# Optimization experiments

Measured on AMD Instinct MI355X. Metric: run time of the kernel, lower is better.

Reference implementation:

```python
import jax, jax.numpy as jnp
import numpy as np

N = 30000
E = 600000
IN = 64
HID = 128
EPS = 1e-5
HEADS_PER_LAYER = (4, 4, 1)


def _bn(x, g, b):
    # eval-mode BatchNorm: running_mean=0, running_var=1
    return x * (g / np.sqrt(1.0 + EPS)) + b


def _segment_softmax(e, dst, n):
    m = jax.ops.segment_max(e, dst, num_segments=n)
    ex = jnp.exp(e - m[dst])
    s = jax.ops.segment_sum(ex, dst, num_segments=n)
    return ex / (s[dst] + 1e-16)


def _gcn_conv(x, w, b, src, dst, norm, n):
    m = (x @ w)[src] * norm[:, None]            # [E+N, HID]
    return jax.ops.segment_sum(m, dst, num_segments=n) + b


def _gat_conv(x, w, a_src, a_dst, b, src, dst, n, heads):
    C = HID // heads
    xh = (x @ w).reshape(n, heads, C)
    asrc = (xh * a_src.reshape(heads, C)).sum(-1)   # [N, heads]
    adst = (xh * a_dst.reshape(heads, C)).sum(-1)
    e = jax.nn.leaky_relu(asrc[src] + adst[dst], 0.2)  # [E+N, heads]
    alpha = _segment_softmax(e, dst, n)
    out = jax.ops.segment_sum(xh[src] * alpha[:, :, None], dst, num_segments=n)
    return out.reshape(n, HID) + b


def _forward(x, gcn_in_w, gcn_in_b, gcn_res_w, gcn_res_b, gcn_w, gcn_b,
             gcn_bn_g, gcn_bn_b, gcn_c1w, gcn_c1b, gcn_c2w, gcn_c2b,
             gcn_c3w, gcn_c3b, gat_in_w, gat_in_b, gat_w, gat_asrc,
             gat_adst, gat_b, gat_bn_g, gat_bn_b, feat_imp, gat_c1w,
             gat_c1b, gat_cbn_g, gat_cbn_b, gat_c2w, gat_c2b, gat_c3w,
             gat_c3b, fin_w, fin_b, fin_bn_g, fin_bn_b, fin2_w, fin2_b,
             edge_index):
    n = x.shape[0]
    loop = jnp.arange(n, dtype=edge_index.dtype)
    src = jnp.concatenate([edge_index[0], loop])  # add self-loops
    dst = jnp.concatenate([edge_index[1], loop])
    # GCN symmetric normalization (with self-loops)
    deg = jax.ops.segment_sum(jnp.ones_like(dst, dtype=x.dtype), dst, num_segments=n)
    dis = jnp.where(deg > 0, jax.lax.rsqrt(jnp.maximum(deg, 1.0)), 0.0)
    norm = dis[src] * dis[dst]

    # ---- GCN branch (eval: dropout = identity, self-attn skipped since N>5000) ----
    xp = x @ gcn_in_w + gcn_in_b
    res = x @ gcn_res_w + gcn_res_b
    for i in range(3):
        xn = _gcn_conv(xp, gcn_w[i], gcn_b[i], src, dst, norm, n)
        xn = jax.nn.relu(_bn(xn, gcn_bn_g[i], gcn_bn_b[i]))
        if i % 2 == 1:
            xp = xn + res
            res = xp
        else:
            xp = xn
    h = jax.nn.relu(xp @ gcn_c1w + gcn_c1b)
    h = jax.nn.relu(h @ gcn_c2w + gcn_c2b)
    gcn_out = h @ gcn_c3w + gcn_c3b

    # ---- GAT branch ----
    xg = x @ gat_in_w + gat_in_b
    for i in range(3):
        xg = _gat_conv(xg, gat_w[i], gat_asrc[i], gat_adst[i], gat_b[i],
                       src, dst, n, HEADS_PER_LAYER[i])
        xg = jax.nn.elu(_bn(xg, gat_bn_g[i], gat_bn_b[i]))
    xg = xg * feat_imp
    h = jax.nn.relu(xg @ gat_c1w + gat_c1b)
    h = _bn(h, gat_cbn_g, gat_cbn_b)
    h = jax.nn.relu(h @ gat_c2w + gat_c2b)
    gat_out = h @ gat_c3w + gat_c3b

    # ---- fusion: N > 10000 -> weighted blend path ----
    fused = 0.6 * gcn_out + 0.4 * gat_out
    h = jax.nn.relu(fused @ fin_w + fin_b)
    h = _bn(h, fin_bn_g, fin_bn_b)
    return h @ fin2_w + fin2_b  # [N, 2]


def setup_inputs() -> dict:
    key = jax.random.key(0)
    ks = iter(jax.random.split(key, 64))

    def nrm(shape, scale=1.0):
        return jax.random.normal(next(ks), shape, dtype=jnp.float32) * scale

    s_in = 1.0 / np.sqrt(IN)
    s_h = 1.0 / np.sqrt(HID)
    inp = {}
    inp['x'] = nrm((N, IN))
    inp['edge_index'] = jax.random.randint(next(ks), (2, E), 0, N, dtype=jnp.int32)
    inp['gcn_in_w'] = nrm((IN, HID), s_in); inp['gcn_in_b'] = nrm((HID,), 0.01)
    inp['gcn_res_w'] = nrm((IN, HID), s_in); inp['gcn_res_b'] = nrm((HID,), 0.01)
    inp['gcn_w'] = nrm((3, HID, HID), s_h); inp['gcn_b'] = nrm((3, HID), 0.01)
    inp['gcn_bn_g'] = 1.0 + nrm((3, HID), 0.1); inp['gcn_bn_b'] = nrm((3, HID), 0.1)
    inp['gcn_c1w'] = nrm((HID, 64), s_h); inp['gcn_c1b'] = nrm((64,), 0.01)
    inp['gcn_c2w'] = nrm((64, 32), 0.125); inp['gcn_c2b'] = nrm((32,), 0.01)
    inp['gcn_c3w'] = nrm((32, HID), 0.18); inp['gcn_c3b'] = nrm((HID,), 0.01)
    inp['gat_in_w'] = nrm((IN, HID), s_in); inp['gat_in_b'] = nrm((HID,), 0.01)
    inp['gat_w'] = nrm((3, HID, HID), s_h)
    inp['gat_asrc'] = nrm((3, HID), s_h); inp['gat_adst'] = nrm((3, HID), s_h)
    inp['gat_b'] = nrm((3, HID), 0.01)
    inp['gat_bn_g'] = 1.0 + nrm((3, HID), 0.1); inp['gat_bn_b'] = nrm((3, HID), 0.1)
    inp['feat_imp'] = 1.0 + nrm((HID,), 0.1)
    inp['gat_c1w'] = nrm((HID, 64), s_h); inp['gat_c1b'] = nrm((64,), 0.01)
    inp['gat_cbn_g'] = 1.0 + nrm((64,), 0.1); inp['gat_cbn_b'] = nrm((64,), 0.1)
    inp['gat_c2w'] = nrm((64, 32), 0.125); inp['gat_c2b'] = nrm((32,), 0.01)
    inp['gat_c3w'] = nrm((32, HID), 0.18); inp['gat_c3b'] = nrm((HID,), 0.01)
    inp['fin_w'] = nrm((HID, 64), s_h); inp['fin_b'] = nrm((64,), 0.01)
    inp['fin_bn_g'] = 1.0 + nrm((64,), 0.1); inp['fin_bn_b'] = nrm((64,), 0.1)
    inp['fin2_w'] = nrm((64, 2), 0.125); inp['fin2_b'] = nrm((2,), 0.01)
    return inp


def reference(x, edge_index, gcn_in_w, gcn_in_b, gcn_res_w, gcn_res_b, gcn_w,
              gcn_b, gcn_bn_g, gcn_bn_b, gcn_c1w, gcn_c1b, gcn_c2w, gcn_c2b,
              gcn_c3w, gcn_c3b, gat_in_w, gat_in_b, gat_w, gat_asrc, gat_adst,
              gat_b, gat_bn_g, gat_bn_b, feat_imp, gat_c1w, gat_c1b, gat_cbn_g,
              gat_cbn_b, gat_c2w, gat_c2b, gat_c3w, gat_c3b, fin_w, fin_b,
              fin_bn_g, fin_bn_b, fin2_w, fin2_b):
    return _forward(x, gcn_in_w, gcn_in_b, gcn_res_w, gcn_res_b, gcn_w, gcn_b,
                    gcn_bn_g, gcn_bn_b, gcn_c1w, gcn_c1b, gcn_c2w, gcn_c2b,
                    gcn_c3w, gcn_c3b, gat_in_w, gat_in_b, gat_w, gat_asrc,
                    gat_adst, gat_b, gat_bn_g, gat_bn_b, feat_imp, gat_c1w,
                    gat_c1b, gat_cbn_g, gat_cbn_b, gat_c2w, gat_c2b, gat_c3w,
                    gat_c3b, fin_w, fin_b, fin_bn_g, fin_bn_b, fin2_w, fin2_b,
                    edge_index)
```

## Files before the change

kernel.cpp:

```cpp
#include <hip/hip_runtime.h>
#include <hip/hip_fp16.h>

#define RSQ_BN 0.9999950000374997f

typedef _Float16 f16x8 __attribute__((ext_vector_type(8)));
typedef float f32x4 __attribute__((ext_vector_type(4)));

union H8u { uint4 u4; __half h[8]; };

__device__ __forceinline__ float leaky02(float x) { return x > 0.f ? x : 0.2f * x; }

__device__ __forceinline__ float4 ld4(const float* p) {
    return *reinterpret_cast<const float4*>(p);
}
__device__ __forceinline__ void st4(float* p, float4 v) {
    *reinterpret_cast<float4*>(p) = v;
}
__device__ __forceinline__ void ld8(float* d, const float* p) {
    float4 u = ld4(p), v = ld4(p + 4);
    d[0] = u.x; d[1] = u.y; d[2] = u.z; d[3] = u.w;
    d[4] = v.x; d[5] = v.y; d[6] = v.z; d[7] = v.w;
}
__device__ __forceinline__ void st8(float* p, const float* v) {
    st4(p, make_float4(v[0], v[1], v[2], v[3]));
    st4(p + 4, make_float4(v[4], v[5], v[6], v[7]));
}


__global__ void hist_k(const int* __restrict__ edst, int* __restrict__ cnt, int E, int EN) {
    int i = blockIdx.x * 256 + threadIdx.x;
    if (i >= EN) return;
    int d = (i < E) ? edst[i] : (i - E);
    atomicAdd(&cnt[d], 1);
}

__global__ __launch_bounds__(256)
void scanA_k(const int* __restrict__ cnt, int* __restrict__ rowptr,
             int* __restrict__ bsum, int n) {
    __shared__ int sh[256];
    int t = threadIdx.x;
    int i = blockIdx.x * 256 + t;
    int v = (i < n) ? cnt[i] : 0;
    sh[t] = v;
    __syncthreads();
#pragma unroll
    for (int off = 1; off < 256; off <<= 1) {
        int u = 0;
        if (t >= off) u = sh[t - off];
        __syncthreads();
        sh[t] += u;
        __syncthreads();
    }
    if (i < n) rowptr[i] = sh[t] - v;
    if (t == 255) bsum[blockIdx.x] = sh[255];
}

__global__ __launch_bounds__(256)
void scanB_k(int* __restrict__ bsum, int nb) {
    __shared__ int sh[256];
    int t = threadIdx.x;
    int v = (t < nb) ? bsum[t] : 0;
    sh[t] = v;
    __syncthreads();
#pragma unroll
    for (int off = 1; off < 256; off <<= 1) {
        int u = 0;
        if (t >= off) u = sh[t - off];
        __syncthreads();
        sh[t] += u;
        __syncthreads();
    }
    if (t < nb) bsum[t] = sh[t] - v;
}

__global__ __launch_bounds__(256)
void scanC_k(const int* __restrict__ cnt, const int* __restrict__ bsum,
             int* __restrict__ rowptr, int* __restrict__ cursor,
             float* __restrict__ dis, int n, int EN) {
    int i = blockIdx.x * 256 + threadIdx.x;
    if (i < n) {
        int r = rowptr[i] + bsum[blockIdx.x];
        rowptr[i] = r;
        cursor[i] = r;
        dis[i] = rsqrtf((float)cnt[i]);
    }
    if (i == 0) rowptr[n] = EN;
}

__global__ void scatter_k(const int* __restrict__ esrc, const int* __restrict__ edst,
                          int* __restrict__ cursor, int* __restrict__ colidx, int E, int EN) {
    int i = blockIdx.x * 256 + threadIdx.x;
    if (i >= EN) return;
    int s, d;
    if (i < E) { s = esrc[i]; d = edst[i]; }
    else       { s = i - E; d = s; }
    int pos = atomicAdd(&cursor[d], 1);
    colidx[pos] = s;
}


__global__ void wtx_all_k(const float* __restrict__ gcn_in_w, const float* __restrict__ gcn_res_w,
                          const float* __restrict__ gat_in_w,
                          const float* __restrict__ gcn_w, const float* __restrict__ gat_w,
                          const float* __restrict__ gcn_c1w, const float* __restrict__ gat_c1w,
                          const float* __restrict__ gcn_c3w, const float* __restrict__ gat_c3w,
                          const float* __restrict__ fin_w,
                          const float* __restrict__ gcn_c2w, const float* __restrict__ gat_c2w,
                          __half* __restrict__ WTin, __half* __restrict__ WTg,
                          __half* __restrict__ WTa, __half* __restrict__ WTc1,
                          __half* __restrict__ WTc3, __half* __restrict__ WTfin,
                          __half* __restrict__ WTc2) {
    int idx = blockIdx.x * 256 + threadIdx.x;
    const float* src;
    __half* dst;
    int K, M, o;
    if (idx < 24576) {
        int mi = idx >> 13; o = idx & 8191;
        src = mi == 0 ? gcn_in_w : (mi == 1 ? gcn_res_w : gat_in_w);
        dst = WTin + mi * 8192; K = 64; M = 128;
    } else if (idx < 73728) {
        int r = idx - 24576; int mi = r >> 14; o = r & 16383;
        src = gcn_w + mi * 16384; dst = WTg + mi * 16384; K = 128; M = 128;
    } else if (idx < 122880) {
        int r = idx - 73728; int mi = r >> 14; o = r & 16383;
        src = gat_w + mi * 16384; dst = WTa + mi * 16384; K = 128; M = 128;
    } else if (idx < 139264) {
        int r = idx - 122880; int mi = r >> 13; o = r & 8191;
        src = mi ? gat_c1w : gcn_c1w; dst = WTc1 + mi * 8192; K = 128; M = 64;
    } else if (idx < 147456) {
        int r = idx - 139264; int mi = r >> 12; o = r & 4095;
        src = mi ? gat_c3w : gcn_c3w; dst = WTc3 + mi * 4096; K = 32; M = 128;
    } else if (idx < 155648) {
        o = idx - 147456; src = fin_w; dst = WTfin; K = 128; M = 64;
    } else if (idx < 159744) {
        int r = idx - 155648; int mi = r >> 11; o = r & 2047;
        src = mi ? gat_c2w : gcn_c2w; dst = WTc2 + mi * 2048; K = 64; M = 32;
    } else return;
    int mcol = o / K, k = o - mcol * K;
    dst[o] = (__half)src[k * M + mcol];
}


__device__ __forceinline__ f16x8 mk_af(const float* xr, int kb) {
    float4 v0 = ld4(xr + kb), v1 = ld4(xr + kb + 4);
    f16x8 af;
    af[0] = (_Float16)v0.x; af[1] = (_Float16)v0.y;
    af[2] = (_Float16)v0.z; af[3] = (_Float16)v0.w;
    af[4] = (_Float16)v1.x; af[5] = (_Float16)v1.y;
    af[6] = (_Float16)v1.z; af[7] = (_Float16)v1.w;
    return af;
}

__global__ __launch_bounds__(256)
void mfma_lin3_k(const float* __restrict__ X, const __half* __restrict__ WTin,
                 const float* __restrict__ b0, float* __restrict__ Y0,
                 const float* __restrict__ b1, float* __restrict__ Y1,
                 const float* __restrict__ b2, float* __restrict__ Y2,
                 int n, int gper) {
    constexpr int K = 64, CT = 8;
    int set = blockIdx.x / gper, blk = blockIdx.x % gper;
    const __half* WT = WTin + (size_t)set * 8192;
    const float* bi = set == 0 ? b0 : (set == 1 ? b1 : b2);
    float* Y = set == 0 ? Y0 : (set == 1 ? Y1 : Y2);
    int wave = threadIdx.x >> 6, lane = threadIdx.x & 63;
    int m = lane & 15, quad = lane >> 4;
    int row0 = blk * 64 + wave * 16;
    int arow = min(row0 + m, n - 1);
    const float* xr = X + (size_t)arow * K;
    f32x4 acc[CT];
#pragma unroll
    for (int ct = 0; ct < CT; ++ct) acc[ct] = (f32x4){0.f, 0.f, 0.f, 0.f};
#pragma unroll
    for (int k32 = 0; k32 < K / 32; ++k32) {
        int kb = k32 * 32 + quad * 8;
        f16x8 af = mk_af(xr, kb);
#pragma unroll
        for (int ct = 0; ct < CT; ++ct) {
            f16x8 bf = *reinterpret_cast<const f16x8*>(WT + (size_t)(ct * 16 + m) * K + kb);
            acc[ct] = __builtin_amdgcn_mfma_f32_16x16x32_f16(af, bf, acc[ct], 0, 0, 0);
        }
    }
#pragma unroll
    for (int ct = 0; ct < CT; ++ct) {
        int col = ct * 16 + m;
        float cb = bi[col];
#pragma unroll
        for (int reg = 0; reg < 4; ++reg) {
            int row = row0 + quad * 4 + reg;
            if (row < n) Y[(size_t)row * 128 + col] = acc[ct][reg] + cb;
        }
    }
}


__global__ __launch_bounds__(256)
void dual128_mfma_k(const float* __restrict__ Xg, const __half* __restrict__ WTg,
                    __half* __restrict__ Yg,
                    const float* __restrict__ Xa, const __half* __restrict__ WTa,
                    __half* __restrict__ Ya,
                    const float* __restrict__ dis,
                    const float* __restrict__ asrc, const float* __restrict__ adst,
                    float* __restrict__ avp, float* __restrict__ bvp,
                    int hh, int n, int gper) {
    bool gat = blockIdx.x >= gper;
    int blk = gat ? blockIdx.x - gper : blockIdx.x;
    const float* X = gat ? Xa : Xg;
    const __half* WT = gat ? WTa : WTg;
    __half* Y = gat ? Ya : Yg;
    int wave = threadIdx.x >> 6;
    int lane = threadIdx.x & 63;
    int m = lane & 15, quad = lane >> 4;
    int row0 = blk * 64 + wave * 16;
    int arow = min(row0 + m, n - 1);
    const float* xr = X + (size_t)arow * 128;
    f32x4 acc[8];
#pragma unroll
    for (int ct = 0; ct < 8; ++ct) acc[ct] = (f32x4){0.f, 0.f, 0.f, 0.f};
#pragma unroll
    for (int k32 = 0; k32 < 4; ++k32) {
        int kb = k32 * 32 + quad * 8;
        f16x8 af = mk_af(xr, kb);
#pragma unroll
        for (int ct = 0; ct < 8; ++ct) {
            f16x8 bf = *reinterpret_cast<const f16x8*>(WT + (size_t)(ct * 16 + m) * 128 + kb);
            acc[ct] = __builtin_amdgcn_mfma_f32_16x16x32_f16(af, bf, acc[ct], 0, 0, 0);
        }
    }
    if (!gat) {
#pragma unroll
        for (int reg = 0; reg < 4; ++reg) {
            int row = row0 + quad * 4 + reg;
            if (row < n) {
                float dv = dis[row];
#pragma unroll
                for (int ct = 0; ct < 8; ++ct)
                    Y[(size_t)row * 128 + ct * 16 + m] = (__half)(acc[ct][reg] * dv);
            }
        }
    } else {
        float cas[8], cad[8];
#pragma unroll
        for (int ct = 0; ct < 8; ++ct) {
            cas[ct] = asrc[ct * 16 + m];
            cad[ct] = adst[ct * 16 + m];
        }
        int ctph = 8 / hh;
#pragma unroll
        for (int reg = 0; reg < 4; ++reg) {
            int row = row0 + quad * 4 + reg;
            bool valid = row < n;
            if (valid) {
#pragma unroll
                for (int ct = 0; ct < 8; ++ct)
                    Y[(size_t)row * 128 + ct * 16 + m] = (__half)acc[ct][reg];
            }
            for (int h = 0; h < hh; ++h) {
                float sa = 0.f, sd = 0.f;
                for (int j = 0; j < ctph; ++j) {
                    int ct = h * ctph + j;
                    sa += acc[ct][reg] * cas[ct];
                    sd += acc[ct][reg] * cad[ct];
                }
                for (int off = 1; off < 16; off <<= 1) {
                    sa += __shfl_xor(sa, off);
                    sd += __shfl_xor(sd, off);
                }
                if (m == 0 && valid) {
                    avp[row * hh + h] = sa;
                    bvp[row * hh + h] = sd;
                }
            }
        }
    }
}


__global__ __launch_bounds__(256)
void fused_gather_k(const int* __restrict__ rowptr, const int* __restrict__ colidx,
                    const float* __restrict__ dis,
                    const __half* __restrict__ Tg, const float* __restrict__ gbias,
                    const float* __restrict__ gbng, const float* __restrict__ gbnb,
                    const float* __restrict__ res, float* __restrict__ Yg,
                    const __half* __restrict__ Ta, const float* __restrict__ avp,
                    const float* __restrict__ bvp, const float* __restrict__ abias,
                    const float* __restrict__ abng, const float* __restrict__ abnb,
                    const float* __restrict__ fimp, float* __restrict__ Ya,
                    int n, int hh, int log2C) {
    int idx = blockIdx.x * 256 + threadIdx.x;
    int i = idx >> 4;
    if (i >= n) return;
    int c = (idx & 15) * 8;
    int h = c >> log2C;
    float ad = bvp[i * hh + h];
    int p0 = rowptr[i], p1 = rowptr[i + 1];
    float g[8], a[8];
#pragma unroll
    for (int t = 0; t < 8; ++t) { g[t] = 0.f; a[t] = 0.f; }
    float m = -3.0e38f, s = 0.f;

    int p = p0;
    int nfull = (p1 - p0) >> 2;
    int sx[4]; float av[4];
    if (nfull > 0) {
#pragma unroll
        for (int j = 0; j < 4; ++j) sx[j] = colidx[p + j];
#pragma unroll
        for (int j = 0; j < 4; ++j) av[j] = avp[sx[j] * hh + h];
    }
    for (int gi = 0; gi < nfull; ++gi) {
        uint4 qg[4], qa[4];
#pragma unroll
        for (int j = 0; j < 4; ++j)
            qg[j] = *reinterpret_cast<const uint4*>(Tg + (size_t)sx[j] * 128 + c);
#pragma unroll
        for (int j = 0; j < 4; ++j)
            qa[j] = *reinterpret_cast<const uint4*>(Ta + (size_t)sx[j] * 128 + c);
        int pn = p + 4;
        bool more = (gi + 1) < nfull;
        int sn[4]; float avn[4];
#pragma unroll
        for (int j = 0; j < 4; ++j) sn[j] = more ? colidx[pn + j] : 0;
#pragma unroll
        for (int j = 0; j < 4; ++j) avn[j] = avp[sn[j] * hh + h];
        float e0 = leaky02(av[0] + ad), e1 = leaky02(av[1] + ad);
        float e2 = leaky02(av[2] + ad), e3 = leaky02(av[3] + ad);
        float mc = fmaxf(fmaxf(e0, e1), fmaxf(e2, e3));
        float mn = fmaxf(m, mc);
        float scale = __expf(m - mn);
        float w0 = __expf(e0 - mn), w1 = __expf(e1 - mn);
        float w2 = __expf(e2 - mn), w3 = __expf(e3 - mn);
        s = s * scale + (w0 + w1 + w2 + w3);
        m = mn;
        {
            H8u k0, k1, k2, k3;
            k0.u4 = qg[0]; k1.u4 = qg[1]; k2.u4 = qg[2]; k3.u4 = qg[3];
#pragma unroll
            for (int t = 0; t < 8; ++t)
                g[t] += __half2float(k0.h[t]) + __half2float(k1.h[t])
                      + __half2float(k2.h[t]) + __half2float(k3.h[t]);
        }
        {
            H8u k0, k1, k2, k3;
            k0.u4 = qa[0]; k1.u4 = qa[1]; k2.u4 = qa[2]; k3.u4 = qa[3];
#pragma unroll
            for (int t = 0; t < 8; ++t) {
                float v = a[t] * scale;
                v = fmaf(__half2float(k0.h[t]), w0, v);
                v = fmaf(__half2float(k1.h[t]), w1, v);
                v = fmaf(__half2float(k2.h[t]), w2, v);
                v = fmaf(__half2float(k3.h[t]), w3, v);
                a[t] = v;
            }
        }
        p = pn;
#pragma unroll
        for (int j = 0; j < 4; ++j) { sx[j] = sn[j]; av[j] = avn[j]; }
    }
    for (; p < p1; ++p) {
        int s0 = colidx[p];
        float e0 = leaky02(avp[s0 * hh + h] + ad);
        uint4 qg0 = *reinterpret_cast<const uint4*>(Tg + (size_t)s0 * 128 + c);
        uint4 qa0 = *reinterpret_cast<const uint4*>(Ta + (size_t)s0 * 128 + c);
        float mn = fmaxf(m, e0);
        float scale = __expf(m - mn);
        float w0 = __expf(e0 - mn);
        s = s * scale + w0;
        m = mn;
        H8u kg, ka; kg.u4 = qg0; ka.u4 = qa0;
#pragma unroll
        for (int t = 0; t < 8; ++t) {
            g[t] += __half2float(kg.h[t]);
            a[t] = fmaf(__half2float(ka.h[t]), w0, a[t] * scale);
        }
    }

    {
        float di = dis[i];
        float bb[8], gg[8], nb[8];
        ld8(bb, gbias + c); ld8(gg, gbng + c); ld8(nb, gbnb + c);
        float o[8];
#pragma unroll
        for (int t = 0; t < 8; ++t) {
            float v = g[t] * di + bb[t];
            o[t] = fmaxf(v * (gg[t] * RSQ_BN) + nb[t], 0.f);
        }
        if (res) {
            float rr[8]; ld8(rr, res + (size_t)i * 128 + c);
#pragma unroll
            for (int t = 0; t < 8; ++t) o[t] += rr[t];
        }
        st8(Yg + (size_t)i * 128 + c, o);
    }
    {
        float si = 1.f / (s + 1e-16f);
        float bb[8], gg[8], nb[8];
        ld8(bb, abias + c); ld8(gg, abng + c); ld8(nb, abnb + c);
        float o[8];
#pragma unroll
        for (int t = 0; t < 8; ++t) {
            float v = a[t] * si + bb[t];
            v = v * (gg[t] * RSQ_BN) + nb[t];
            o[t] = v > 0.f ? v : expm1f(v);
        }
        if (fimp) {
            float ff[8]; ld8(ff, fimp + c);
#pragma unroll
            for (int t = 0; t < 8; ++t) o[t] *= ff[t];
        }
        st8(Ya + (size_t)i * 128 + c, o);
    }
}


__global__ __launch_bounds__(256)
void fused_tail_k(const float* __restrict__ Xg, const float* __restrict__ Xa,
                  const __half* __restrict__ WTc1,
                  const float* __restrict__ c1bg, const float* __restrict__ c1ba,
                  const float* __restrict__ cbng, const float* __restrict__ cbnb,
                  const __half* __restrict__ WTc2,
                  const float* __restrict__ c2bg, const float* __restrict__ c2ba,
                  const __half* __restrict__ WTc3,
                  const float* __restrict__ c3bg, const float* __restrict__ c3ba,
                  const __half* __restrict__ WTfin, const float* __restrict__ finb,
                  const float* __restrict__ fbng, const float* __restrict__ fbnb,
                  const float* __restrict__ w2, const float* __restrict__ b2,
                  float* __restrict__ out, int n) {
    __shared__ alignas(16) __half h1s[2][64][88];
    __shared__ alignas(16) __half h2s[2][64][56];
    __shared__ alignas(16) __half Fs[64][152];
    int wave = threadIdx.x >> 6, lane = threadIdx.x & 63;
    int m = lane & 15, quad = lane >> 4;
    int row0 = blockIdx.x * 64 + wave * 16;
    int lr0 = wave * 16;
    int arow = min(row0 + m, n - 1);

#pragma unroll
    for (int br = 0; br < 2; ++br) {
        const float* xr = (br ? Xa : Xg) + (size_t)arow * 128;
        const __half* WT = WTc1 + br * 8192;
        f32x4 acc[4];
#pragma unroll
        for (int ct = 0; ct < 4; ++ct) acc[ct] = (f32x4){0.f, 0.f, 0.f, 0.f};
#pragma unroll
        for (int k32 = 0; k32 < 4; ++k32) {
            int kb = k32 * 32 + quad * 8;
            f16x8 af = mk_af(xr, kb);
#pragma unroll
            for (int ct = 0; ct < 4; ++ct) {
                f16x8 bf = *reinterpret_cast<const f16x8*>(WT + (ct * 16 + m) * 128 + kb);
                acc[ct] = __builtin_amdgcn_mfma_f32_16x16x32_f16(af, bf, acc[ct], 0, 0, 0);
            }
        }
        const float* bi = br ? c1ba : c1bg;
#pragma unroll
        for (int ct = 0; ct < 4; ++ct) {
            int col = ct * 16 + m;
            float cb = bi[col];
            float cg = br ? cbng[col] * RSQ_BN : 1.f;
            float cbb = br ? cbnb[col] : 0.f;
#pragma unroll
            for (int reg = 0; reg < 4; ++reg) {
                float v = fmaxf(acc[ct][reg] + cb, 0.f) * cg + cbb;
                h1s[br][lr0 + quad * 4 + reg][col] = (__half)v;
            }
        }
    }
    __syncthreads();
#pragma unroll
    for (int br = 0; br < 2; ++br) {
        f32x4 acc[2];
        acc[0] = (f32x4){0.f, 0.f, 0.f, 0.f};
        acc[1] = (f32x4){0.f, 0.f, 0.f, 0.f};
        const __half* WT = WTc2 + br * 2048;
#pragma unroll
        for (int k32 = 0; k32 < 2; ++k32) {
            int kb = k32 * 32 + quad * 8;
            f16x8 af = *reinterpret_cast<const f16x8*>(&h1s[br][lr0 + m][kb]);
#pragma unroll
            for (int ct = 0; ct < 2; ++ct) {
                f16x8 bf = *reinterpret_cast<const f16x8*>(WT + (ct * 16 + m) * 64 + kb);
                acc[ct] = __builtin_amdgcn_mfma_f32_16x16x32_f16(af, bf, acc[ct], 0, 0, 0);
            }
        }
        const float* bi = br ? c2ba : c2bg;
#pragma unroll
        for (int ct = 0; ct < 2; ++ct) {
            int col = ct * 16 + m;
            float cb = bi[col];
#pragma unroll
            for (int reg = 0; reg < 4; ++reg) {
                float v = fmaxf(acc[ct][reg] + cb, 0.f);
                h2s[br][lr0 + quad * 4 + reg][col] = (__half)v;
            }
        }
    }
    __syncthreads();
    {
        f32x4 ag[8], aa[8];
#pragma unroll
        for (int ct = 0; ct < 8; ++ct) {
            ag[ct] = (f32x4){0.f, 0.f, 0.f, 0.f};
            aa[ct] = (f32x4){0.f, 0.f, 0.f, 0.f};
        }
        int kb = quad * 8;
        f16x8 afg = *reinterpret_cast<const f16x8*>(&h2s[0][lr0 + m][kb]);
        f16x8 afa = *reinterpret_cast<const f16x8*>(&h2s[1][lr0 + m][kb]);
#pragma unroll
        for (int ct = 0; ct < 8; ++ct) {
            f16x8 bfg = *reinterpret_cast<const f16x8*>(WTc3 + (ct * 16 + m) * 32 + kb);
            f16x8 bfa = *reinterpret_cast<const f16x8*>(WTc3 + 4096 + (ct * 16 + m) * 32 + kb);
            ag[ct] = __builtin_amdgcn_mfma_f32_16x16x32_f16(afg, bfg, ag[ct], 0, 0, 0);
            aa[ct] = __builtin_amdgcn_mfma_f32_16x16x32_f16(afa, bfa, aa[ct], 0, 0, 0);
        }
#pragma unroll
        for (int ct = 0; ct < 8; ++ct) {
            int col = ct * 16 + m;
            float cb = 0.6f * c3bg[col] + 0.4f * c3ba[col];
#pragma unroll
            for (int reg = 0; reg < 4; ++reg) {
                float v = 0.6f * ag[ct][reg] + 0.4f * aa[ct][reg] + cb;
                Fs[lr0 + quad * 4 + reg][col] = (__half)v;
            }
        }
    }
    __syncthreads();
    {
        f32x4 acc[4];
#pragma unroll
        for (int ct = 0; ct < 4; ++ct) acc[ct] = (f32x4){0.f, 0.f, 0.f, 0.f};
#pragma unroll
        for (int k32 = 0; k32 < 4; ++k32) {
            int kb = k32 * 32 + quad * 8;
            f16x8 af = *reinterpret_cast<const f16x8*>(&Fs[lr0 + m][kb]);
#pragma unroll
            for (int ct = 0; ct < 4; ++ct) {
                f16x8 bf = *reinterpret_cast<const f16x8*>(WTfin + (ct * 16 + m) * 128 + kb);
                acc[ct] = __builtin_amdgcn_mfma_f32_16x16x32_f16(af, bf, acc[ct], 0, 0, 0);
            }
        }
        float p0[4] = {0.f, 0.f, 0.f, 0.f}, p1[4] = {0.f, 0.f, 0.f, 0.f};
#pragma unroll
        for (int ct = 0; ct < 4; ++ct) {
            int col = ct * 16 + m;
            float cb = finb[col];
            float cg = fbng[col] * RSQ_BN;
            float cbb = fbnb[col];
            float w20 = w2[2 * col], w21 = w2[2 * col + 1];
#pragma unroll
            for (int reg = 0; reg < 4; ++reg) {
                float v = fmaxf(acc[ct][reg] + cb, 0.f) * cg + cbb;
                p0[reg] += v * w20;
                p1[reg] += v * w21;
            }
        }
        for (int off = 1; off < 16; off <<= 1) {
#pragma unroll
            for (int reg = 0; reg < 4; ++reg) {
                p0[reg] += __shfl_xor(p0[reg], off);
                p1[reg] += __shfl_xor(p1[reg], off);
            }
        }
        if (m == 0) {
#pragma unroll
            for (int reg = 0; reg < 4; ++reg) {
                int row = row0 + quad * 4 + reg;
                if (row < n) {
                    out[row * 2] = p0[reg] + b2[0];
                    out[row * 2 + 1] = p1[reg] + b2[1];
                }
            }
        }
    }
}


static inline int cdiv(int a, int b) { return (a + b - 1) / b; }

extern "C" void kernel_launch(void* const* d_in, const int* in_sizes, int n_in,
                              void* d_out, int out_size, void* d_ws, size_t ws_size,
                              hipStream_t stream) {
    const float* x       = (const float*)d_in[0];
    const int*   ei      = (const int*)d_in[1];
    const float* gcn_in_w = (const float*)d_in[2];
    const float* gcn_in_b = (const float*)d_in[3];
    const float* gcn_res_w = (const float*)d_in[4];
    const float* gcn_res_b = (const float*)d_in[5];
    const float* gcn_w   = (const float*)d_in[6];
    const float* gcn_b   = (const float*)d_in[7];
    const float* gcn_bn_g = (const float*)d_in[8];
    const float* gcn_bn_b = (const float*)d_in[9];
    const float* gcn_c1w = (const float*)d_in[10];
    const float* gcn_c1b = (const float*)d_in[11];
    const float* gcn_c2w = (const float*)d_in[12];
    const float* gcn_c2b = (const float*)d_in[13];
    const float* gcn_c3w = (const float*)d_in[14];
    const float* gcn_c3b = (const float*)d_in[15];
    const float* gat_in_w = (const float*)d_in[16];
    const float* gat_in_b = (const float*)d_in[17];
    const float* gat_w   = (const float*)d_in[18];
    const float* gat_asrc = (const float*)d_in[19];
    const float* gat_adst = (const float*)d_in[20];
    const float* gat_b   = (const float*)d_in[21];
    const float* gat_bn_g = (const float*)d_in[22];
    const float* gat_bn_b = (const float*)d_in[23];
    const float* feat_imp = (const float*)d_in[24];
    const float* gat_c1w = (const float*)d_in[25];
    const float* gat_c1b = (const float*)d_in[26];
    const float* gat_cbn_g = (const float*)d_in[27];
    const float* gat_cbn_b = (const float*)d_in[28];
    const float* gat_c2w = (const float*)d_in[29];
    const float* gat_c2b = (const float*)d_in[30];
    const float* gat_c3w = (const float*)d_in[31];
    const float* gat_c3b = (const float*)d_in[32];
    const float* fin_w   = (const float*)d_in[33];
    const float* fin_b   = (const float*)d_in[34];
    const float* fin_bn_g = (const float*)d_in[35];
    const float* fin_bn_b = (const float*)d_in[36];
    const float* fin2_w  = (const float*)d_in[37];
    const float* fin2_b  = (const float*)d_in[38];

    const int N = in_sizes[0] / 64;
    const int E = in_sizes[1] / 2;
    const int EN = E + N;
    const int* esrc = ei;
    const int* edst = ei + E;

    char* wp = (char*)d_ws;
    auto alloc = [&](size_t bytes) -> void* {
        void* p = (void*)wp;
        wp += (bytes + 255) & ~(size_t)255;
        return p;
    };
    int* cnt    = (int*)alloc((size_t)N * 4);
    int* rowptr = (int*)alloc((size_t)(N + 1) * 4);
    int* cursor = (int*)alloc((size_t)N * 4);
    int* bsum   = (int*)alloc((size_t)256 * 4);
    int* colidx = (int*)alloc((size_t)EN * 4);
    float* dis  = (float*)alloc((size_t)N * 4);
    float* A    = (float*)alloc((size_t)N * 128 * 4);
    float* B    = (float*)alloc((size_t)N * 128 * 4);
    float* G    = (float*)alloc((size_t)N * 128 * 4);
    float* H    = (float*)alloc((size_t)N * 128 * 4);
    float* R    = (float*)alloc((size_t)N * 128 * 4);
    __half* Th1 = (__half*)alloc((size_t)N * 128 * 2);
    __half* Th2 = (__half*)alloc((size_t)N * 128 * 2);
    float* avv  = (float*)alloc((size_t)N * 4 * 4);
    float* bvv  = (float*)alloc((size_t)N * 4 * 4);
    __half* WTin = (__half*)alloc((size_t)3 * 8192 * 2);
    __half* WTg  = (__half*)alloc((size_t)3 * 16384 * 2);
    __half* WTa  = (__half*)alloc((size_t)3 * 16384 * 2);
    __half* WTc1 = (__half*)alloc((size_t)2 * 8192 * 2);
    __half* WTc3 = (__half*)alloc((size_t)2 * 4096 * 2);
    __half* WTfin = (__half*)alloc((size_t)8192 * 2);
    __half* WTc2 = (__half*)alloc((size_t)2 * 2048 * 2);

    const int nScanB = cdiv(N, 256);
    hipMemsetAsync(cnt, 0, (size_t)N * 4, stream);
    hist_k<<<cdiv(EN, 256), 256, 0, stream>>>(edst, cnt, E, EN);
    scanA_k<<<nScanB, 256, 0, stream>>>(cnt, rowptr, bsum, N);
    scanB_k<<<1, 256, 0, stream>>>(bsum, nScanB);
    scanC_k<<<nScanB, 256, 0, stream>>>(cnt, bsum, rowptr, cursor, dis, N, EN);
    scatter_k<<<cdiv(EN, 256), 256, 0, stream>>>(esrc, edst, cursor, colidx, E, EN);
    wtx_all_k<<<624, 256, 0, stream>>>(gcn_in_w, gcn_res_w, gat_in_w, gcn_w, gat_w,
                                       gcn_c1w, gat_c1w, gcn_c3w, gat_c3w, fin_w,
                                       gcn_c2w, gat_c2w,
                                       WTin, WTg, WTa, WTc1, WTc3, WTfin, WTc2);

    const int g64r = cdiv(N, 64);
    const int gG   = cdiv(N, 16);

    mfma_lin3_k<<<3 * g64r, 256, 0, stream>>>(x, WTin, gcn_in_b, A, gcn_res_b, R,
                                              gat_in_b, G, N, g64r);

    const int heads_arr[3] = {4, 4, 1};
    float* gcur = A; float* gnxt = B;
    float* acur = G; float* anxt = H;
    for (int i = 0; i < 3; ++i) {
        int hh = heads_arr[i];
        int log2C = (hh == 4) ? 5 : 7;
        dual128_mfma_k<<<2 * g64r, 256, 0, stream>>>(gcur, WTg + (size_t)i * 16384, Th1,
                                                     acur, WTa + (size_t)i * 16384, Th2, dis,
                                                     gat_asrc + i * 128, gat_adst + i * 128,
                                                     avv, bvv, hh, N, g64r);
        fused_gather_k<<<gG, 256, 0, stream>>>(rowptr, colidx, dis,
                                               Th1, gcn_b + i * 128, gcn_bn_g + i * 128,
                                               gcn_bn_b + i * 128, (i == 1) ? R : nullptr, gnxt,
                                               Th2, avv, bvv, gat_b + i * 128,
                                               gat_bn_g + i * 128, gat_bn_b + i * 128,
                                               (i == 2) ? feat_imp : nullptr, anxt,
                                               N, hh, log2C);
        float* t = gcur; gcur = gnxt; gnxt = t;
        t = acur; acur = anxt; anxt = t;
    }

    fused_tail_k<<<g64r, 256, 0, stream>>>(gcur, acur,
                                           WTc1, gcn_c1b, gat_c1b, gat_cbn_g, gat_cbn_b,
                                           WTc2, gcn_c2b, gat_c2b,
                                           WTc3, gcn_c3b, gat_c3b,
                                           WTfin, fin_b, fin_bn_g, fin_bn_b,
                                           fin2_w, fin2_b, (float*)d_out, N);
}
```

Before: 481.0 us.

## Split gather edges across two lanes, fold attention vectors into weights, single-kernel scan

Three changes. First, the three-kernel prefix scan is merged into one single-block kernel of 1024 threads, each scanning a contiguous chunk. Second, the GAT attention projections are precomputed as W·a_src and W·a_dst, stored as extra fp16 weight columns, and computed with one extra MFMA instead of per-row shuffle reductions; this adds fp16 rounding to the attention logits. Third, the fused gather kernel splits each node's edge list between two 16-lane halves and merges their online-softmax states with shuffles, doubling parallelism for the edge-bound gather.

```diff
diff --git a/kernel.cpp b/kernel.cpp
--- a/kernel.cpp
+++ b/kernel.cpp
@@ -34,57 +34,33 @@
     atomicAdd(&cnt[d], 1);
 }
 
-__global__ __launch_bounds__(256)
-void scanA_k(const int* __restrict__ cnt, int* __restrict__ rowptr,
-             int* __restrict__ bsum, int n) {
-    __shared__ int sh[256];
+__global__ __launch_bounds__(1024)
+void scan_all_k(const int* __restrict__ cnt, int* __restrict__ rowptr,
+                int* __restrict__ cursor, float* __restrict__ dis, int n, int EN) {
+    __shared__ int sh[1024];
     int t = threadIdx.x;
-    int i = blockIdx.x * 256 + t;
-    int v = (i < n) ? cnt[i] : 0;
-    sh[t] = v;
+    int ch = (n + 1023) >> 10;
+    int b = t * ch, e = min(b + ch, n);
+    int sum = 0;
+    for (int i = b; i < e; ++i) sum += cnt[i];
+    sh[t] = sum;
     __syncthreads();
 #pragma unroll
-    for (int off = 1; off < 256; off <<= 1) {
-        int u = 0;
-        if (t >= off) u = sh[t - off];
+    for (int off = 1; off < 1024; off <<= 1) {
+        int u = (t >= off) ? sh[t - off] : 0;
         __syncthreads();
         sh[t] += u;
         __syncthreads();
     }
-    if (i < n) rowptr[i] = sh[t] - v;
-    if (t == 255) bsum[blockIdx.x] = sh[255];
-}
-
-__global__ __launch_bounds__(256)
-void scanB_k(int* __restrict__ bsum, int nb) {
-    __shared__ int sh[256];
-    int t = threadIdx.x;
-    int v = (t < nb) ? bsum[t] : 0;
-    sh[t] = v;
-    __syncthreads();
-#pragma unroll
-    for (int off = 1; off < 256; off <<= 1) {
-        int u = 0;
-        if (t >= off) u = sh[t - off];
-        __syncthreads();
-        sh[t] += u;
-        __syncthreads();
-    }
-    if (t < nb) bsum[t] = sh[t] - v;
-}
-
-__global__ __launch_bounds__(256)
-void scanC_k(const int* __restrict__ cnt, const int* __restrict__ bsum,
-             int* __restrict__ rowptr, int* __restrict__ cursor,
-             float* __restrict__ dis, int n, int EN) {
-    int i = blockIdx.x * 256 + threadIdx.x;
-    if (i < n) {
-        int r = rowptr[i] + bsum[blockIdx.x];
-        rowptr[i] = r;
-        cursor[i] = r;
-        dis[i] = rsqrtf((float)cnt[i]);
-    }
-    if (i == 0) rowptr[n] = EN;
+    int run = sh[t] - sum;
+    for (int i = b; i < e; ++i) {
+        int c = cnt[i];
+        rowptr[i] = run;
+        cursor[i] = run;
+        dis[i] = rsqrtf((float)c);
+        run += c;
+    }
+    if (t == 0) rowptr[n] = EN;
 }
 
 __global__ void scatter_k(const int* __restrict__ esrc, const int* __restrict__ edst,
@@ -106,10 +82,11 @@
                           const float* __restrict__ gcn_c3w, const float* __restrict__ gat_c3w,
                           const float* __restrict__ fin_w,
                           const float* __restrict__ gcn_c2w, const float* __restrict__ gat_c2w,
+                          const float* __restrict__ gat_asrc, const float* __restrict__ gat_adst,
                           __half* __restrict__ WTin, __half* __restrict__ WTg,
                           __half* __restrict__ WTa, __half* __restrict__ WTc1,
                           __half* __restrict__ WTc3, __half* __restrict__ WTfin,
-                          __half* __restrict__ WTc2) {
+                          __half* __restrict__ WTc2, __half* __restrict__ WTd) {
     int idx = blockIdx.x * 256 + threadIdx.x;
     const float* src;
     __half* dst;
@@ -135,6 +112,25 @@
     } else if (idx < 159744) {
         int r = idx - 155648; int mi = r >> 11; o = r & 2047;
         src = mi ? gat_c2w : gcn_c2w; dst = WTc2 + mi * 2048; K = 64; M = 32;
+    } else if (idx < 165888) {
+        int r = idx - 159744;
+        int layer = r >> 11; o = r & 2047;
+        int col = o >> 7, k = o & 127;
+        int hh = (layer < 2) ? 4 : 1;
+        int C = 128 / hh;
+        float v = 0.f;
+        if (col < hh) {
+            const float* w = gat_w + (size_t)(layer * 128 + k) * 128 + col * C;
+            const float* av = gat_asrc + layer * 128 + col * C;
+            for (int c2 = 0; c2 < C; ++c2) v += w[c2] * av[c2];
+        } else if (col >= 8 && col < 8 + hh) {
+            int hthis = col - 8;
+            const float* w = gat_w + (size_t)(layer * 128 + k) * 128 + hthis * C;
+            const float* av = gat_adst + layer * 128 + hthis * C;
+            for (int c2 = 0; c2 < C; ++c2) v += w[c2] * av[c2];
+        }
+        WTd[(size_t)layer * 2048 + o] = (__half)v;
+        return;
     } else return;
     int mcol = o / K, k = o - mcol * K;
     dst[o] = (__half)src[k * M + mcol];
@@ -199,7 +195,7 @@
                     const float* __restrict__ Xa, const __half* __restrict__ WTa,
                     __half* __restrict__ Ya,
                     const float* __restrict__ dis,
-                    const float* __restrict__ asrc, const float* __restrict__ adst,
+                    const __half* __restrict__ WTd,
                     float* __restrict__ avp, float* __restrict__ bvp,
                     int hh, int n, int gper) {
     bool gat = blockIdx.x >= gper;
@@ -216,17 +212,17 @@
     f32x4 acc[8];
 #pragma unroll
     for (int ct = 0; ct < 8; ++ct) acc[ct] = (f32x4){0.f, 0.f, 0.f, 0.f};
-#pragma unroll
-    for (int k32 = 0; k32 < 4; ++k32) {
-        int kb = k32 * 32 + quad * 8;
-        f16x8 af = mk_af(xr, kb);
-#pragma unroll
-        for (int ct = 0; ct < 8; ++ct) {
-            f16x8 bf = *reinterpret_cast<const f16x8*>(WT + (size_t)(ct * 16 + m) * 128 + kb);
-            acc[ct] = __builtin_amdgcn_mfma_f32_16x16x32_f16(af, bf, acc[ct], 0, 0, 0);
-        }
-    }
     if (!gat) {
+#pragma unroll
+        for (int k32 = 0; k32 < 4; ++k32) {
+            int kb = k32 * 32 + quad * 8;
+            f16x8 af = mk_af(xr, kb);
+#pragma unroll
+            for (int ct = 0; ct < 8; ++ct) {
+                f16x8 bf = *reinterpret_cast<const f16x8*>(WT + (size_t)(ct * 16 + m) * 128 + kb);
+                acc[ct] = __builtin_amdgcn_mfma_f32_16x16x32_f16(af, bf, acc[ct], 0, 0, 0);
+            }
+        }
 #pragma unroll
         for (int reg = 0; reg < 4; ++reg) {
             int row = row0 + quad * 4 + reg;
@@ -238,37 +234,28 @@
             }
         }
     } else {
-        float cas[8], cad[8];
-#pragma unroll
-        for (int ct = 0; ct < 8; ++ct) {
-            cas[ct] = asrc[ct * 16 + m];
-            cad[ct] = adst[ct * 16 + m];
-        }
-        int ctph = 8 / hh;
+        f32x4 accd = (f32x4){0.f, 0.f, 0.f, 0.f};
+#pragma unroll
+        for (int k32 = 0; k32 < 4; ++k32) {
+            int kb = k32 * 32 + quad * 8;
+            f16x8 af = mk_af(xr, kb);
+#pragma unroll
+            for (int ct = 0; ct < 8; ++ct) {
+                f16x8 bf = *reinterpret_cast<const f16x8*>(WT + (size_t)(ct * 16 + m) * 128 + kb);
+                acc[ct] = __builtin_amdgcn_mfma_f32_16x16x32_f16(af, bf, acc[ct], 0, 0, 0);
+            }
+            f16x8 bd = *reinterpret_cast<const f16x8*>(WTd + (size_t)m * 128 + kb);
+            accd = __builtin_amdgcn_mfma_f32_16x16x32_f16(af, bd, accd, 0, 0, 0);
+        }
 #pragma unroll
         for (int reg = 0; reg < 4; ++reg) {
             int row = row0 + quad * 4 + reg;
-            bool valid = row < n;
-            if (valid) {
+            if (row < n) {
 #pragma unroll
                 for (int ct = 0; ct < 8; ++ct)
                     Y[(size_t)row * 128 + ct * 16 + m] = (__half)acc[ct][reg];
-            }
-            for (int h = 0; h < hh; ++h) {
-                float sa = 0.f, sd = 0.f;
-                for (int j = 0; j < ctph; ++j) {
-                    int ct = h * ctph + j;
-                    sa += acc[ct][reg] * cas[ct];
-                    sd += acc[ct][reg] * cad[ct];
-                }
-                for (int off = 1; off < 16; off <<= 1) {
-                    sa += __shfl_xor(sa, off);
-                    sd += __shfl_xor(sd, off);
-                }
-                if (m == 0 && valid) {
-                    avp[row * hh + h] = sa;
-                    bvp[row * hh + h] = sd;
-                }
+                if (m < hh) avp[row * hh + m] = accd[reg];
+                else if (m >= 8 && m < 8 + hh) bvp[row * hh + (m - 8)] = accd[reg];
             }
         }
     }
@@ -287,12 +274,16 @@
                     const float* __restrict__ fimp, float* __restrict__ Ya,
                     int n, int hh, int log2C) {
     int idx = blockIdx.x * 256 + threadIdx.x;
-    int i = idx >> 4;
+    int i = idx >> 5;
     if (i >= n) return;
+    int half = (idx >> 4) & 1;
     int c = (idx & 15) * 8;
     int h = c >> log2C;
     float ad = bvp[i * hh + h];
-    int p0 = rowptr[i], p1 = rowptr[i + 1];
+    int q0 = rowptr[i], q1 = rowptr[i + 1];
+    int cnt0 = (q1 - q0 + 1) >> 1;
+    int p0 = half ? q0 + cnt0 : q0;
+    int p1 = half ? q1 : q0 + cnt0;
     float g[8], a[8];
 #pragma unroll
     for (int t = 0; t < 8; ++t) { g[t] = 0.f; a[t] = 0.f; }
@@ -373,6 +364,22 @@
             a[t] = fmaf(__half2float(ka.h[t]), w0, a[t] * scale);
         }
     }
+
+    {
+        float m2 = __shfl_xor(m, 16);
+        float s2 = __shfl_xor(s, 16);
+        float mn = fmaxf(m, m2);
+        float wA = __expf(m - mn), wB = __expf(m2 - mn);
+        s = s * wA + s2 * wB;
+#pragma unroll
+        for (int t = 0; t < 8; ++t) {
+            float g2 = __shfl_xor(g[t], 16);
+            float a2 = __shfl_xor(a[t], 16);
+            g[t] += g2;
+            a[t] = a[t] * wA + a2 * wB;
+        }
+    }
+    if (half) return;
 
     {
         float di = dis[i];
@@ -634,7 +641,6 @@
     int* cnt    = (int*)alloc((size_t)N * 4);
     int* rowptr = (int*)alloc((size_t)(N + 1) * 4);
     int* cursor = (int*)alloc((size_t)N * 4);
-    int* bsum   = (int*)alloc((size_t)256 * 4);
     int* colidx = (int*)alloc((size_t)EN * 4);
     float* dis  = (float*)alloc((size_t)N * 4);
     float* A    = (float*)alloc((size_t)N * 128 * 4);
@@ -653,21 +659,19 @@
     __half* WTc3 = (__half*)alloc((size_t)2 * 4096 * 2);
     __half* WTfin = (__half*)alloc((size_t)8192 * 2);
     __half* WTc2 = (__half*)alloc((size_t)2 * 2048 * 2);
-
-    const int nScanB = cdiv(N, 256);
+    __half* WTd  = (__half*)alloc((size_t)3 * 2048 * 2);
+
     hipMemsetAsync(cnt, 0, (size_t)N * 4, stream);
     hist_k<<<cdiv(EN, 256), 256, 0, stream>>>(edst, cnt, E, EN);
-    scanA_k<<<nScanB, 256, 0, stream>>>(cnt, rowptr, bsum, N);
-    scanB_k<<<1, 256, 0, stream>>>(bsum, nScanB);
-    scanC_k<<<nScanB, 256, 0, stream>>>(cnt, bsum, rowptr, cursor, dis, N, EN);
+    scan_all_k<<<1, 1024, 0, stream>>>(cnt, rowptr, cursor, dis, N, EN);
     scatter_k<<<cdiv(EN, 256), 256, 0, stream>>>(esrc, edst, cursor, colidx, E, EN);
-    wtx_all_k<<<624, 256, 0, stream>>>(gcn_in_w, gcn_res_w, gat_in_w, gcn_w, gat_w,
+    wtx_all_k<<<648, 256, 0, stream>>>(gcn_in_w, gcn_res_w, gat_in_w, gcn_w, gat_w,
                                        gcn_c1w, gat_c1w, gcn_c3w, gat_c3w, fin_w,
-                                       gcn_c2w, gat_c2w,
-                                       WTin, WTg, WTa, WTc1, WTc3, WTfin, WTc2);
+                                       gcn_c2w, gat_c2w, gat_asrc, gat_adst,
+                                       WTin, WTg, WTa, WTc1, WTc3, WTfin, WTc2, WTd);
 
     const int g64r = cdiv(N, 64);
-    const int gG   = cdiv(N, 16);
+    const int gG   = cdiv(N, 8);
 
     mfma_lin3_k<<<3 * g64r, 256, 0, stream>>>(x, WTin, gcn_in_b, A, gcn_res_b, R,
                                               gat_in_b, G, N, g64r);
@@ -680,7 +684,7 @@
         int log2C = (hh == 4) ? 5 : 7;
         dual128_mfma_k<<<2 * g64r, 256, 0, stream>>>(gcur, WTg + (size_t)i * 16384, Th1,
                                                      acur, WTa + (size_t)i * 16384, Th2, dis,
-                                                     gat_asrc + i * 128, gat_adst + i * 128,
+                                                     WTd + (size_t)i * 2048,
                                                      avv, bvv, hh, N, g64r);
         fused_gather_k<<<gG, 256, 0, stream>>>(rowptr, colidx, dis,
                                                Th1, gcn_b + i * 128, gcn_bn_g + i * 128,
```

Measured after the change: 546.9 us. +13.7%, slower.
